# Kernel optimization log

Measured on AMD Instinct MI355X. Metric: run time of the kernel, lower is better.

The kernel has to match this reference:

```python
import jax, jax.numpy as jnp
import numpy as np

B, C, D, H, W = 8, 96, 8, 32, 32
HW, DIM, NH = H * W, C * D, 4
DH = DIM // NH
EPS_NORM = 1e-12
EPS_LN = 1e-5


def setup_inputs() -> dict:
    key = jax.random.key(0)
    ks = jax.random.split(key, 10)
    s = 0.02
    return {
        "x": jax.random.normal(ks[0], (B, C, D, H, W), jnp.float32),
        "pos_embed": jax.random.normal(ks[1], (1, HW, DIM), jnp.float32) * s,
        "qkv_w": jax.random.normal(ks[2], (3 * DIM, DIM), jnp.float32) * s,
        "proj_w": jax.random.normal(ks[3], (DIM, DIM), jnp.float32) * s,
        "proj_b": jnp.zeros((DIM,), jnp.float32),
        "temperature": jnp.ones((NH, 1, 1), jnp.float32),
        "ln_gamma": jnp.ones((DIM,), jnp.float32),
        "ln_beta": jnp.zeros((DIM,), jnp.float32),
        "dw_w": jax.random.normal(ks[4], (C, 1, 3, 3, 3), jnp.float32) * s,
        "dw_b": jnp.zeros((C,), jnp.float32),
        "pw_w": jax.random.normal(ks[5], (C, C, 1, 1, 1), jnp.float32) * s,
        "pw_b": jnp.zeros((C,), jnp.float32),
    }


def _l2norm_seq(t):
    # normalize over the HW axis (dim=-2), matching F.normalize(dim=-2)
    n = jnp.sqrt(jnp.sum(t * t, axis=-2, keepdims=True))
    return t / jnp.maximum(n, EPS_NORM)


def _dsconv(y, dw_w, dw_b, pw_w, pw_b):
    dn = ("NCDHW", "OIDHW", "NCDHW")
    z = jax.lax.conv_general_dilated(y, dw_w, (1, 1, 1), [(1, 1)] * 3,
                                     dimension_numbers=dn, feature_group_count=C)
    z = z + dw_b[None, :, None, None, None]
    z = jax.lax.conv_general_dilated(z, pw_w, (1, 1, 1), [(0, 0)] * 3,
                                     dimension_numbers=dn)
    return z + pw_b[None, :, None, None, None]


def reference(x, pos_embed, qkv_w, proj_w, proj_b, temperature,
              ln_gamma, ln_beta, dw_w, dw_b, pw_w, pw_b):
    save = x
    # b c d h w -> b (h w) (c d)
    t = jnp.transpose(x, (0, 3, 4, 1, 2)).reshape(B, HW, DIM)
    t = t + pos_embed
    # qkv projection (no bias)
    qkv = (t @ qkv_w.T).reshape(B, HW, 3, NH, DH)
    qkv = jnp.transpose(qkv, (2, 0, 3, 1, 4))  # [3,B,NH,HW,DH]
    q, k, v = qkv[0], qkv[1], qkv[2]
    q = _l2norm_seq(q)
    k = _l2norm_seq(k)
    attn = jnp.einsum("bhnd,bhmd->bhnm", q, k) * temperature  # temp broadcasts [NH,1,1]
    attn = jax.nn.softmax(attn, axis=-1)  # dropout = identity at eval
    o = jnp.einsum("bhnm,bhmd->bhnd", attn, v)
    o = jnp.transpose(o, (0, 2, 1, 3)).reshape(B, HW, DIM)
    o = o @ proj_w.T + proj_b
    # LayerNorm applied to attention output
    mu = jnp.mean(o, axis=-1, keepdims=True)
    var = jnp.mean((o - mu) ** 2, axis=-1, keepdims=True)
    o = (o - mu) / jnp.sqrt(var + EPS_LN) * ln_gamma + ln_beta
    # b (h w) (c d) -> b c d h w
    o = o.reshape(B, H, W, C, D)
    o = jnp.transpose(o, (0, 3, 4, 1, 2))
    y = o + save
    return y + _dsconv(y, dw_w, dw_b, pw_w, pw_b)
```

## Files before the change

kernel.cpp:

```cpp
#include <hip/hip_runtime.h>

typedef unsigned short u16;
typedef unsigned int u32;

typedef __attribute__((ext_vector_type(8))) short short8;
typedef __attribute__((ext_vector_type(4))) float floatx4;

__device__ __forceinline__ float bf2f(u16 u) { return __uint_as_float(((u32)u) << 16); }
__device__ __forceinline__ u16 f2bf(float f) {
    u32 x = __float_as_uint(f);
    x += 0x7fffu + ((x >> 16) & 1u);
    return (u16)(x >> 16);
}
__device__ __forceinline__ void gl_lds16(const void* g, void* l) {
    __builtin_amdgcn_global_load_lds((const __attribute__((address_space(1))) u32*)g,
                                     (__attribute__((address_space(3))) u32*)l, 16, 0, 0);
}


__global__ __launch_bounds__(256) void k_tpos(const float* __restrict__ x,
                                              const float* __restrict__ pos,
                                              u16* __restrict__ t) {
    __shared__ float tile[64][65];
    const int b = blockIdx.z, hw0 = blockIdx.y * 64, cd0 = blockIdx.x * 64;
    const int tid = threadIdx.x;
#pragma unroll
    for (int i = 0; i < 16; i++) {
        int f = i * 256 + tid;
        int cdl = f >> 6, hwl = f & 63;
        int cd = cd0 + cdl, c = cd >> 3, d = cd & 7;
        tile[cdl][hwl] = x[(size_t)(((b * 96 + c) * 8 + d)) * 1024 + hw0 + hwl];
    }
    __syncthreads();
#pragma unroll
    for (int it = 0; it < 2; it++) {
        int u = it * 256 + tid;
        int ch = u >> 6, l = u & 63;
        int n16l = ch >> 1, kcl = ch & 1;
        int hwl = n16l * 16 + (l & 15);
        int cdl = kcl * 32 + (l >> 4) * 8;
        int row = b * 1024 + hw0 + hwl;
        int cd = cd0 + cdl;
        const float* pp = pos + (size_t)(hw0 + hwl) * 768 + cd;
        float4 p0 = *(const float4*)pp;
        float4 p1 = *(const float4*)(pp + 4);
        short8 v;
        v[0] = (short)f2bf(tile[cdl + 0][hwl] + p0.x);
        v[1] = (short)f2bf(tile[cdl + 1][hwl] + p0.y);
        v[2] = (short)f2bf(tile[cdl + 2][hwl] + p0.z);
        v[3] = (short)f2bf(tile[cdl + 3][hwl] + p0.w);
        v[4] = (short)f2bf(tile[cdl + 4][hwl] + p1.x);
        v[5] = (short)f2bf(tile[cdl + 5][hwl] + p1.y);
        v[6] = (short)f2bf(tile[cdl + 6][hwl] + p1.z);
        v[7] = (short)f2bf(tile[cdl + 7][hwl] + p1.w);
        size_t chunk = (size_t)(row >> 4) * 24 + (cd >> 5);
        *(short8*)(t + chunk * 512 + l * 8) = v;
    }
}

__global__ __launch_bounds__(256) void k_cvt(const float* __restrict__ wq,
                                             const float* __restrict__ wp,
                                             const float* __restrict__ wpw,
                                             u16* __restrict__ out) {
    const int NQ = 144 * 24 * 64;
    const int NP = NQ + 48 * 24 * 64;
    int u = blockIdx.x * 256 + threadIdx.x;
    if (u < NP) {
        const float* w = (u < NQ) ? wq : wp;
        int ub = (u < NQ) ? u : u - NQ;
        int chunk = ub >> 6, l = ub & 63;
        int n16 = chunk / 24, kc = chunk - n16 * 24;
        int n = n16 * 16 + (l & 15);
        int k0 = kc * 32 + (l >> 4) * 8;
        const float* src = w + (size_t)n * 768 + k0;
        float4 a = *(const float4*)src;
        float4 b2 = *(const float4*)(src + 4);
        short8 v;
        v[0] = (short)f2bf(a.x);  v[1] = (short)f2bf(a.y);
        v[2] = (short)f2bf(a.z);  v[3] = (short)f2bf(a.w);
        v[4] = (short)f2bf(b2.x); v[5] = (short)f2bf(b2.y);
        v[6] = (short)f2bf(b2.z); v[7] = (short)f2bf(b2.w);
        *(short8*)(out + (size_t)u * 8) = v;
    } else {
        int i = u - NP;
        out[(size_t)NP * 8 + i] = f2bf(wpw[i]);
    }
}

template <int MODE>
__global__ __launch_bounds__(256) void gemm_bt(const u16* __restrict__ A,
                                               const u16* __restrict__ Bw,
                                               int M, int N, int K,
                                               u16* __restrict__ qo, u16* __restrict__ ko,
                                               u16* __restrict__ vo,
                                               const float* __restrict__ bias,
                                               float* __restrict__ Co) {
    __shared__ __align__(16) u16 lAB[32 * 512];
    u16* lA = lAB;
    u16* lB = lAB + 16 * 512;
    const int tid = threadIdx.x;
    const int lane = tid & 63;
    const int wv = tid >> 6;
    const int wr = wv >> 1, wc = wv & 1;
    const int ntiles = N >> 7;
    const int mtiles = M >> 7;
    const int lin = blockIdx.x;
    const int xcd = lin & 7;
    const int idx = lin >> 3;
    const int mlocal = idx / ntiles;
    const int ntile = idx - mlocal * ntiles;
    const int m0 = (xcd * (mtiles >> 3) + mlocal) << 7;
    const int n0 = ntile << 7;
    const int lr = lane & 15;
    const int lq = lane >> 4;

    floatx4 acc[4][4];
#pragma unroll
    for (int i = 0; i < 4; i++)
#pragma unroll
        for (int j = 0; j < 4; j++) acc[i][j] = (floatx4){0.f, 0.f, 0.f, 0.f};

    const int m16 = m0 >> 4, n16 = n0 >> 4;
    for (int kc2 = 0; kc2 < (K >> 6); kc2++) {
        __syncthreads();
#pragma unroll
        for (int kh = 0; kh < 2; kh++) {
#pragma unroll
            for (int i = 0; i < 2; i++) {
                int ch16 = i * 4 + wv;
                int kc = kc2 * 2 + kh;
                const u16* ga = A + ((size_t)(m16 + ch16) * 24 + kc) * 512 + lane * 8;
                gl_lds16(ga, (char*)lA + (kh * 8 + ch16) * 1024);
                const u16* gb = Bw + ((size_t)(n16 + ch16) * 24 + kc) * 512 + lane * 8;
                gl_lds16(gb, (char*)lB + (kh * 8 + ch16) * 1024);
            }
        }
        __syncthreads();
#pragma unroll
        for (int kh = 0; kh < 2; kh++) {
            short8 af[4], bfr[4];
#pragma unroll
            for (int tt = 0; tt < 4; tt++) {
                af[tt] = *(const short8*)(lA + ((kh * 8 + wr * 4 + tt) * 64 + lane) * 8);
                bfr[tt] = *(const short8*)(lB + ((kh * 8 + wc * 4 + tt) * 64 + lane) * 8);
            }
#pragma unroll
            for (int mt = 0; mt < 4; mt++)
#pragma unroll
                for (int nt = 0; nt < 4; nt++)
                    acc[mt][nt] = __builtin_amdgcn_mfma_f32_16x16x32_bf16(af[mt], bfr[nt], acc[mt][nt], 0, 0, 0);
        }
    }

    if (MODE == 0) {
        const int region = n0 / 768;
        const int n0r = n0 - region * 768;
        if (region == 0) {
#pragma unroll
            for (int nt = 0; nt < 4; nt++) {
                int colb = n0r + wc * 64 + nt * 16;
                int h = colb / 192;
                int dh = colb - h * 192 + lr;
#pragma unroll
                for (int mt = 0; mt < 4; mt++) {
#pragma unroll
                    for (int r = 0; r < 4; r++) {
                        int row = m0 + wr * 64 + mt * 16 + lq * 4 + r;
                        int b = row >> 10, n = row & 1023;
                        qo[((size_t)(b * 4 + h) * 1024 + n) * 192 + dh] = f2bf(acc[mt][nt][r]);
                    }
                }
            }
        } else {
            __syncthreads();
            if (region == 1) {
#pragma unroll
                for (int nt = 0; nt < 4; nt++) {
                    int lch = wc * 2 + (nt >> 1);
                    int offbase = (((nt & 1) * 2 + (lr >> 3)) * 16) * 8 + (lr & 7);
#pragma unroll
                    for (int mt = 0; mt < 4; mt++) {
                        u16* cp2 = lAB + (((wr * 4 + mt) * 4 + lch) * 512);
#pragma unroll
                        for (int r = 0; r < 4; r++)
                            cp2[offbase + (lq * 4 + r) * 8] = f2bf(acc[mt][nt][r]);
                    }
                }
            } else {
#pragma unroll
                for (int nt = 0; nt < 4; nt++) {
#pragma unroll
                    for (int mt = 0; mt < 4; mt++) {
                        u16* cp2 = lAB + (((wr * 2 + (mt >> 1)) * 8 + wc * 4 + nt) * 512);
                        int ob = (((mt & 1) * 2 + (lq >> 1)) * 16 + lr) * 8 + (lq & 1) * 4;
#pragma unroll
                        for (int r = 0; r < 4; r++)
                            cp2[ob + r] = f2bf(acc[mt][nt][r]);
                    }
                }
            }
            __syncthreads();
            const int b = m0 >> 10;
            const int ml = m0 & 1023;
#pragma unroll
            for (int i = 0; i < 8; i++) {
                int ci = wv * 8 + i;
                short8 val = *(const short8*)(lAB + ci * 512 + lane * 8);
                if (region == 1) {
                    int a = ci >> 2, bb = ci & 3;
                    int cg = n0r + bb * 32;
                    int h = cg / 192;
                    int dh32 = (cg - h * 192) >> 5;
                    size_t gaddr = (size_t)(b * 4 + h) * 196608 +
                                   (size_t)((((ml >> 4) + a) * 6 + dh32)) * 512 + lane * 8;
                    *(short8*)(ko + gaddr) = val;
                } else {
                    int a = ci >> 3, bb = ci & 7;
                    int cg = n0r + bb * 16;
                    int h = cg / 192;
                    int dh16 = (cg - h * 192) >> 4;
                    size_t gaddr = (size_t)(b * 4 + h) * 196608 +
                                   (size_t)((((ml >> 5) + a) * 12 + dh16)) * 512 + lane * 8;
                    *(short8*)(vo + gaddr) = val;
                }
            }
        }
    } else {
#pragma unroll
        for (int nt = 0; nt < 4; nt++) {
            int col = n0 + wc * 64 + nt * 16 + lr;
            float bv = bias[col];
#pragma unroll
            for (int mt = 0; mt < 4; mt++) {
#pragma unroll
                for (int r = 0; r < 4; r++) {
                    int row = m0 + wr * 64 + mt * 16 + lq * 4 + r;
                    Co[(size_t)row * N + col] = acc[mt][nt][r] + bv;
                }
            }
        }
    }
}

__global__ void k_sq(const u16* __restrict__ q, const u16* __restrict__ k,
                     float* __restrict__ sqq, float* __restrict__ sqk) {
    int bh = blockIdx.x;
    int part = blockIdx.y;
    int dh = threadIdx.x;
    const u16* qp = q + ((size_t)bh * 1024 + part * 128) * 192 + dh;
    float aq = 0.f;
#pragma unroll 4
    for (int n = 0; n < 128; n++) {
        float a = bf2f(qp[(size_t)n * 192]);
        aq += a * a;
    }
    const u16* kbase = k + (size_t)bh * 196608 + (dh >> 5) * 512 + ((dh >> 3) & 3) * 128 + (dh & 7);
    float ak = 0.f;
#pragma unroll 4
    for (int n = 0; n < 128; n++) {
        int nn = part * 128 + n;
        float c2 = bf2f(kbase[(nn >> 4) * 3072 + (nn & 15) * 8]);
        ak += c2 * c2;
    }
    atomicAdd(&sqq[bh * 192 + dh], aq);
    atomicAdd(&sqk[bh * 192 + dh], ak);
}

__global__ void k_scale(const float* __restrict__ sqq, const float* __restrict__ sqk,
                        const float* __restrict__ temp, float* __restrict__ cs) {
    int bh = blockIdx.x;
    int dh = threadIdx.x;
    float rq = 1.f / fmaxf(sqrtf(sqq[bh * 192 + dh]), 1e-12f);
    float rk = 1.f / fmaxf(sqrtf(sqk[bh * 192 + dh]), 1e-12f);
    cs[bh * 192 + dh] = rq * rk * temp[bh & 3];
}

__global__ __launch_bounds__(256) void k_attn(const u16* __restrict__ q,
                                              const u16* __restrict__ kmat,
                                              const u16* __restrict__ vT,
                                              const float* __restrict__ cs,
                                              u16* __restrict__ o) {
    __shared__ __align__(16) u16 lK[24 * 512];
    __shared__ __align__(16) u16 lV[24 * 512];
    __shared__ __align__(16) u16 lP[4 * 1024];
    const int lin = blockIdx.x;
    const int qb = (lin >> 3) & 15;
    const int bh = (lin & 7) * 4 + (lin >> 7);
    const int b = bh >> 2, h = bh & 3;
    const int tid = threadIdx.x;
    const int lane = tid & 63;
    const int wv = tid >> 6;
    const int lr = lane & 15;
    const int lq = lane >> 4;
    const int koff = lq * 8;

    const u16* qbase = q + (size_t)bh * 1024 * 192;
    const u16* kbase = kmat + (size_t)bh * 196608;
    const u16* vbase = vT + (size_t)bh * 196608;
    const float* cp = cs + bh * 192;

    const int qrow = qb * 64 + wv * 16 + lr;
    const u16* qp = qbase + (size_t)qrow * 192;
    short8 qf[6];
#pragma unroll
    for (int ks = 0; ks < 6; ks++) {
        short8 raw = *(const short8*)(qp + ks * 32 + koff);
        short8 sc;
#pragma unroll
        for (int j = 0; j < 8; j++) {
            float f = bf2f((u16)raw[j]) * cp[ks * 32 + koff + j];
            sc[j] = (short)f2bf(f);
        }
        qf[ks] = sc;
    }

    float m_r[4], l_r[4];
    floatx4 oacc[12];
#pragma unroll
    for (int r = 0; r < 4; r++) { m_r[r] = -1e30f; l_r[r] = 0.f; }
#pragma unroll
    for (int vt = 0; vt < 12; vt++) oacc[vt] = (floatx4){0.f, 0.f, 0.f, 0.f};

    u16* lp = lP + wv * 1024;

    for (int kb = 0; kb < 16; kb++) {
        __syncthreads();
#pragma unroll
        for (int i = 0; i < 6; i++) {
            int ch = i * 4 + wv;
            int ks = ch >> 2, nt = ch & 3;
            const u16* gk = kbase + ((size_t)(kb * 4 + nt) * 6 + ks) * 512 + lane * 8;
            gl_lds16(gk, (char*)lK + ch * 1024);
            int ks2 = ch / 12, vt2 = ch - ks2 * 12;
            const u16* gv = vbase + ((size_t)(kb * 2 + ks2) * 12 + vt2) * 512 + lane * 8;
            gl_lds16(gv, (char*)lV + ch * 1024);
        }
        __syncthreads();

        floatx4 s[4];
#pragma unroll
        for (int nt = 0; nt < 4; nt++) s[nt] = (floatx4){0.f, 0.f, 0.f, 0.f};
#pragma unroll
        for (int ks = 0; ks < 6; ks++) {
#pragma unroll
            for (int nt = 0; nt < 4; nt++) {
                short8 kf = *(const short8*)(lK + ((ks * 4 + nt) * 64 + lane) * 8);
                s[nt] = __builtin_amdgcn_mfma_f32_16x16x32_bf16(qf[ks], kf, s[nt], 0, 0, 0);
            }
        }

        float rmax[4];
#pragma unroll
        for (int r = 0; r < 4; r++)
            rmax[r] = fmaxf(fmaxf(s[0][r], s[1][r]), fmaxf(s[2][r], s[3][r]));
#pragma unroll
        for (int m = 1; m < 16; m <<= 1)
#pragma unroll
            for (int r = 0; r < 4; r++) rmax[r] = fmaxf(rmax[r], __shfl_xor(rmax[r], m));
        float alpha[4];
#pragma unroll
        for (int r = 0; r < 4; r++) {
            float mn = fmaxf(m_r[r], rmax[r]);
            alpha[r] = __expf(m_r[r] - mn);
            m_r[r] = mn;
        }
        float rsum[4] = {0.f, 0.f, 0.f, 0.f};
#pragma unroll
        for (int nt = 0; nt < 4; nt++)
#pragma unroll
            for (int r = 0; r < 4; r++) {
                float p = __expf(s[nt][r] - m_r[r]);
                s[nt][r] = p;
                rsum[r] += p;
            }
#pragma unroll
        for (int m = 1; m < 16; m <<= 1)
#pragma unroll
            for (int r = 0; r < 4; r++) rsum[r] += __shfl_xor(rsum[r], m);
#pragma unroll
        for (int r = 0; r < 4; r++) l_r[r] = l_r[r] * alpha[r] + rsum[r];
#pragma unroll
        for (int vt = 0; vt < 12; vt++)
#pragma unroll
            for (int r = 0; r < 4; r++) oacc[vt][r] *= alpha[r];

#pragma unroll
        for (int nt = 0; nt < 4; nt++) {
            int base2 = (nt >> 1) * 512 + ((nt & 1) * 2 + (lr >> 3)) * 128 + (lr & 7);
#pragma unroll
            for (int r = 0; r < 4; r++)
                lp[base2 + (lq * 4 + r) * 8] = f2bf(s[nt][r]);
        }

#pragma unroll
        for (int ks2 = 0; ks2 < 2; ks2++) {
            short8 pf = *(const short8*)(lp + ks2 * 512 + lane * 8);
#pragma unroll
            for (int vt = 0; vt < 12; vt++) {
                short8 vf = *(const short8*)(lV + ((ks2 * 12 + vt) * 64 + lane) * 8);
                oacc[vt] = __builtin_amdgcn_mfma_f32_16x16x32_bf16(pf, vf, oacc[vt], 0, 0, 0);
            }
        }
    }

    float inv[4];
#pragma unroll
    for (int r = 0; r < 4; r++) inv[r] = 1.f / l_r[r];
#pragma unroll
    for (int vt = 0; vt < 12; vt++) {
        int col = h * 192 + vt * 16 + lr;
#pragma unroll
        for (int r = 0; r < 4; r++) {
            int rowg = b * 1024 + qb * 64 + wv * 16 + lq * 4 + r;
            size_t addr = (size_t)(rowg >> 4) * 12288 + (col >> 5) * 512 +
                          ((col >> 3) & 3) * 128 + (rowg & 15) * 8 + (col & 7);
            o[addr] = f2bf(oacc[vt][r] * inv[r]);
        }
    }
}

__global__ __launch_bounds__(256) void k_lnstats(const float* __restrict__ o2,
                                                 float* __restrict__ mu,
                                                 float* __restrict__ rstd) {
    int row = blockIdx.x;
    int tid = threadIdx.x;
    const float* p = o2 + (size_t)row * 768;
    float s = 0.f, ss = 0.f;
    for (int i = tid; i < 768; i += 256) {
        float v = p[i];
        s += v;
        ss += v * v;
    }
#pragma unroll
    for (int m = 32; m >= 1; m >>= 1) {
        s += __shfl_xor(s, m);
        ss += __shfl_xor(ss, m);
    }
    __shared__ float as[4], ass[4];
    if ((tid & 63) == 0) {
        as[tid >> 6] = s;
        ass[tid >> 6] = ss;
    }
    __syncthreads();
    if (tid == 0) {
        float S = as[0] + as[1] + as[2] + as[3];
        float SS = ass[0] + ass[1] + ass[2] + ass[3];
        float m_ = S * (1.f / 768.f);
        float v = SS * (1.f / 768.f) - m_ * m_;
        v = fmaxf(v, 0.f);
        mu[row] = m_;
        rstd[row] = rsqrtf(v + 1e-5f);
    }
}

__global__ __launch_bounds__(256) void k_lnt(const float* __restrict__ o2,
                                             const float* __restrict__ mu,
                                             const float* __restrict__ rstd,
                                             const float* __restrict__ gamma,
                                             const float* __restrict__ beta,
                                             const float* __restrict__ x,
                                             float* __restrict__ y) {
    __shared__ float tile[64][65];
    const int b = blockIdx.z, hw0 = blockIdx.y * 64, cd0 = blockIdx.x * 64;
    const int tid = threadIdx.x;
#pragma unroll
    for (int i = 0; i < 16; i++) {
        int f = i * 256 + tid;
        int hwl = f >> 6, cdl = f & 63;
        int row = b * 1024 + hw0 + hwl;
        float v = o2[(size_t)row * 768 + cd0 + cdl];
        v = (v - mu[row]) * rstd[row] * gamma[cd0 + cdl] + beta[cd0 + cdl];
        tile[hwl][cdl] = v;
    }
    __syncthreads();
#pragma unroll
    for (int i = 0; i < 16; i++) {
        int f = i * 256 + tid;
        int cdl = f >> 6, hwl = f & 63;
        int cd = cd0 + cdl, c = cd >> 3, d = cd & 7;
        size_t addr = (size_t)((b * 96 + c) * 8 + d) * 1024 + hw0 + hwl;
        y[addr] = tile[hwl][cdl] + x[addr];
    }
}

__global__ __launch_bounds__(256) void k_dw(const float* __restrict__ y,
                                            const float* __restrict__ w,
                                            const float* __restrict__ bias,
                                            float* __restrict__ z) {
    __shared__ float ly[8192];
    const int bc = blockIdx.x;
    const int c = bc % 96;
    const int tid = threadIdx.x;
    const size_t base = (size_t)bc * 8192;

#pragma unroll
    for (int i = 0; i < 8; i++) {
        int i4 = i * 256 + tid;
        *(float4*)(ly + i4 * 4) = *(const float4*)(y + base + i4 * 4);
    }
    float wt[27];
#pragma unroll
    for (int j = 0; j < 27; j++) wt[j] = w[c * 27 + j];
    const float bv = bias[c];
    __syncthreads();

    const int wcol = tid & 31;
    const int hh = tid >> 5;

    for (int hb = 0; hb < 4; hb++) {
        const int h = hb * 8 + hh;
        float pl[3][9];
        auto loadplane = [&](int dd, float* p) {
#pragma unroll
            for (int kh = 0; kh < 3; kh++) {
                int h2 = h + kh - 1;
                bool hok = (unsigned)h2 < 32u;
                const float* row = ly + dd * 1024 + h2 * 32;
#pragma unroll
                for (int kw = 0; kw < 3; kw++) {
                    int w2 = wcol + kw - 1;
                    bool ok = hok && (unsigned)w2 < 32u;
                    p[kh * 3 + kw] = ok ? row[w2] : 0.f;
                }
            }
        };
#pragma unroll
        for (int j = 0; j < 9; j++) pl[0][j] = 0.f;
        loadplane(0, pl[1]);
#pragma unroll
        for (int d = 0; d < 8; d++) {
            if (d < 7) loadplane(d + 1, pl[2]);
            else {
#pragma unroll
                for (int j = 0; j < 9; j++) pl[2][j] = 0.f;
            }
            float acc = bv;
#pragma unroll
            for (int kd = 0; kd < 3; kd++)
#pragma unroll
                for (int j = 0; j < 9; j++) acc += wt[kd * 9 + j] * pl[kd][j];
            z[base + d * 1024 + h * 32 + wcol] = acc;
#pragma unroll
            for (int j = 0; j < 9; j++) { pl[0][j] = pl[1][j]; pl[1][j] = pl[2][j]; }
        }
    }
}

__global__ __launch_bounds__(256) void k_pw(const float* __restrict__ z,
                                            const u16* __restrict__ wbf,
                                            const float* __restrict__ bias,
                                            float* __restrict__ out) {
    __shared__ __align__(16) u16 lZ[128 * 104];
    __shared__ __align__(16) u16 lW[96 * 104];
    const int tid = threadIdx.x;
    const int lane = tid & 63;
    const int wv = tid >> 6;
    const int lr = lane & 15;
    const int lq = lane >> 4;
    const int koff = lq * 8;

    const int idx = blockIdx.x;
    const int q = idx & 7;
    const int bd = idx >> 3;
    const int b = bd >> 3, d = bd & 7;
    const int pos0 = q * 128;

    for (int i = tid; i < 96 * 96; i += 256) {
        int row = i / 96, col = i - row * 96;
        lW[row * 104 + col] = wbf[i];
    }
    {
        const int pos = tid & 127;
        const int cc0 = (tid >> 7) * 48;
        const size_t gbase = ((size_t)b * 96 * 8 + d) * 1024 + pos0 + pos;
#pragma unroll
        for (int g = 0; g < 6; g++) {
            short8 v;
#pragma unroll
            for (int j = 0; j < 8; j++) {
                int cc = cc0 + g * 8 + j;
                v[j] = (short)f2bf(z[gbase + (size_t)cc * 8192]);
            }
            *(short8*)(lZ + pos * 104 + cc0 + g * 8) = v;
        }
    }
    __syncthreads();

    floatx4 acc[6][2];
#pragma unroll
    for (int m = 0; m < 6; m++)
#pragma unroll
        for (int nt = 0; nt < 2; nt++) acc[m][nt] = (floatx4){0.f, 0.f, 0.f, 0.f};

#pragma unroll
    for (int ks = 0; ks < 3; ks++) {
        short8 bfrg[2];
#pragma unroll
        for (int nt = 0; nt < 2; nt++)
            bfrg[nt] = *(const short8*)(lZ + (wv * 32 + nt * 16 + lr) * 104 + ks * 32 + koff);
#pragma unroll
        for (int m = 0; m < 6; m++) {
            short8 afr = *(const short8*)(lW + (m * 16 + lr) * 104 + ks * 32 + koff);
#pragma unroll
            for (int nt = 0; nt < 2; nt++)
                acc[m][nt] = __builtin_amdgcn_mfma_f32_16x16x32_bf16(afr, bfrg[nt], acc[m][nt], 0, 0, 0);
        }
    }

#pragma unroll
    for (int m = 0; m < 6; m++) {
#pragma unroll
        for (int r = 0; r < 4; r++) {
            int c = m * 16 + lq * 4 + r;
            float bv = bias[c];
            size_t rowbase = ((size_t)(b * 96 + c) * 8 + d) * 1024 + pos0;
#pragma unroll
            for (int nt = 0; nt < 2; nt++) {
                int pos = wv * 32 + nt * 16 + lr;
                size_t a = rowbase + pos;
                out[a] = out[a] + bv + acc[m][nt][r];
            }
        }
    }
}

extern "C" void kernel_launch(void* const* d_in, const int* in_sizes, int n_in,
                              void* d_out, int out_size, void* d_ws, size_t ws_size,
                              hipStream_t stream) {
    (void)in_sizes; (void)n_in; (void)out_size; (void)ws_size;
    const float* x      = (const float*)d_in[0];
    const float* pos    = (const float*)d_in[1];
    const float* qkv_w  = (const float*)d_in[2];
    const float* proj_w = (const float*)d_in[3];
    const float* proj_b = (const float*)d_in[4];
    const float* temp   = (const float*)d_in[5];
    const float* ln_g   = (const float*)d_in[6];
    const float* ln_b   = (const float*)d_in[7];
    const float* dw_w   = (const float*)d_in[8];
    const float* dw_b   = (const float*)d_in[9];
    const float* pw_w   = (const float*)d_in[10];
    const float* pw_b   = (const float*)d_in[11];
    float* out = (float*)d_out;
    char* ws = (char*)d_ws;

    u16* t    = (u16*)(ws + 0);
    u16* vT   = (u16*)(ws + 12582912);
    u16* q    = (u16*)(ws + 25165824);
    u16* kk   = (u16*)(ws + 37748736);
    u16* wqb  = (u16*)(ws + 50331648);
    float* cs   = (float*)(ws + 55150592);
    float* sqq  = (float*)(ws + 55175168);
    float* sqk  = (float*)(ws + 55199744);
    float* mu   = (float*)(ws + 55224320);
    float* rstd = (float*)(ws + 55257088);
    u16* wpb  = wqb + 2304 * 768;
    u16* wpwb = wqb + 2304 * 768 + 768 * 768;
    u16* o   = t;
    float* o2 = (float*)q;
    float* z  = (float*)t;
    float* y  = out;

    k_tpos<<<dim3(12, 16, 8), 256, 0, stream>>>(x, pos, t);
    k_cvt<<<1188, 256, 0, stream>>>(qkv_w, proj_w, pw_w, wqb);
    gemm_bt<0><<<1152, 256, 0, stream>>>(t, wqb, 8192, 2304, 768, q, kk, vT, nullptr, nullptr);
    hipMemsetAsync(sqq, 0, 49152, stream);
    k_sq<<<dim3(32, 8), 192, 0, stream>>>(q, kk, sqq, sqk);
    k_scale<<<32, 192, 0, stream>>>(sqq, sqk, temp, cs);
    k_attn<<<512, 256, 0, stream>>>(q, kk, vT, cs, o);
    gemm_bt<1><<<384, 256, 0, stream>>>(o, wpb, 8192, 768, 768, nullptr, nullptr, nullptr, proj_b, o2);
    k_lnstats<<<8192, 256, 0, stream>>>(o2, mu, rstd);
    k_lnt<<<dim3(12, 16, 8), 256, 0, stream>>>(o2, mu, rstd, ln_g, ln_b, x, y);
    k_dw<<<768, 256, 0, stream>>>(y, dw_w, dw_b, z);
    k_pw<<<512, 256, 0, stream>>>(z, wpwb, pw_b, out);
}
```

Measured before the change: 295.2 us.

## Process two query tiles per wave in attention and drop online max rescaling

The attention kernel now runs with 128 threads per block, and each wave handles 32 query rows as two 16-row tiles. Every K and V fragment read from LDS therefore feeds two MFMAs, which halves LDS fragment traffic per unit of compute. The online-softmax running max and the alpha rescaling of accumulators are removed, and scores are exponentiated directly. This relies on normalized q/k keeping scores small enough not to overflow exp, which is a numerical risk if temperature or scores grow large. Register pressure rises, since two sets of accumulators are live, and fewer waves per block may reduce latency hiding.

```diff
diff --git a/kernel.cpp b/kernel.cpp
--- a/kernel.cpp
+++ b/kernel.cpp
@@ -275,14 +275,14 @@
     cs[bh * 192 + dh] = rq * rk * temp[bh & 3];
 }
 
-__global__ __launch_bounds__(256) void k_attn(const u16* __restrict__ q,
+__global__ __launch_bounds__(128) void k_attn(const u16* __restrict__ q,
                                               const u16* __restrict__ kmat,
                                               const u16* __restrict__ vT,
                                               const float* __restrict__ cs,
                                               u16* __restrict__ o) {
     __shared__ __align__(16) u16 lK[24 * 512];
     __shared__ __align__(16) u16 lV[24 * 512];
-    __shared__ __align__(16) u16 lP[4 * 1024];
+    __shared__ __align__(16) u16 lP[2 * 2048];
     const int lin = blockIdx.x;
     const int qb = (lin >> 3) & 15;
     const int bh = (lin & 7) * 4 + (lin >> 7);
@@ -299,35 +299,41 @@
     const u16* vbase = vT + (size_t)bh * 196608;
     const float* cp = cs + bh * 192;
 
-    const int qrow = qb * 64 + wv * 16 + lr;
-    const u16* qp = qbase + (size_t)qrow * 192;
-    short8 qf[6];
-#pragma unroll
-    for (int ks = 0; ks < 6; ks++) {
-        short8 raw = *(const short8*)(qp + ks * 32 + koff);
-        short8 sc;
-#pragma unroll
-        for (int j = 0; j < 8; j++) {
-            float f = bf2f((u16)raw[j]) * cp[ks * 32 + koff + j];
-            sc[j] = (short)f2bf(f);
-        }
-        qf[ks] = sc;
-    }
-
-    float m_r[4], l_r[4];
-    floatx4 oacc[12];
-#pragma unroll
-    for (int r = 0; r < 4; r++) { m_r[r] = -1e30f; l_r[r] = 0.f; }
-#pragma unroll
-    for (int vt = 0; vt < 12; vt++) oacc[vt] = (floatx4){0.f, 0.f, 0.f, 0.f};
-
-    u16* lp = lP + wv * 1024;
+    short8 qf[2][6];
+#pragma unroll
+    for (int t = 0; t < 2; t++) {
+        const int qrow = qb * 64 + wv * 32 + t * 16 + lr;
+        const u16* qp = qbase + (size_t)qrow * 192;
+#pragma unroll
+        for (int ks = 0; ks < 6; ks++) {
+            short8 raw = *(const short8*)(qp + ks * 32 + koff);
+            short8 sc;
+#pragma unroll
+            for (int j = 0; j < 8; j++) {
+                float f = bf2f((u16)raw[j]) * cp[ks * 32 + koff + j];
+                sc[j] = (short)f2bf(f);
+            }
+            qf[t][ks] = sc;
+        }
+    }
+
+    float l_r[2][4];
+    floatx4 oacc[2][12];
+#pragma unroll
+    for (int t = 0; t < 2; t++) {
+#pragma unroll
+        for (int r = 0; r < 4; r++) l_r[t][r] = 0.f;
+#pragma unroll
+        for (int vt = 0; vt < 12; vt++) oacc[t][vt] = (floatx4){0.f, 0.f, 0.f, 0.f};
+    }
+
+    u16* lp = lP + wv * 2048;
 
     for (int kb = 0; kb < 16; kb++) {
         __syncthreads();
 #pragma unroll
-        for (int i = 0; i < 6; i++) {
-            int ch = i * 4 + wv;
+        for (int i = 0; i < 12; i++) {
+            int ch = i * 2 + wv;
             int ks = ch >> 2, nt = ch & 3;
             const u16* gk = kbase + ((size_t)(kb * 4 + nt) * 6 + ks) * 512 + lane * 8;
             gl_lds16(gk, (char*)lK + ch * 1024);
@@ -337,84 +343,84 @@
         }
         __syncthreads();
 
-        floatx4 s[4];
-#pragma unroll
-        for (int nt = 0; nt < 4; nt++) s[nt] = (floatx4){0.f, 0.f, 0.f, 0.f};
+        floatx4 s0[4], s1[4];
+#pragma unroll
+        for (int nt = 0; nt < 4; nt++) {
+            s0[nt] = (floatx4){0.f, 0.f, 0.f, 0.f};
+            s1[nt] = (floatx4){0.f, 0.f, 0.f, 0.f};
+        }
 #pragma unroll
         for (int ks = 0; ks < 6; ks++) {
 #pragma unroll
             for (int nt = 0; nt < 4; nt++) {
                 short8 kf = *(const short8*)(lK + ((ks * 4 + nt) * 64 + lane) * 8);
-                s[nt] = __builtin_amdgcn_mfma_f32_16x16x32_bf16(qf[ks], kf, s[nt], 0, 0, 0);
-            }
-        }
-
-        float rmax[4];
-#pragma unroll
-        for (int r = 0; r < 4; r++)
-            rmax[r] = fmaxf(fmaxf(s[0][r], s[1][r]), fmaxf(s[2][r], s[3][r]));
+                s0[nt] = __builtin_amdgcn_mfma_f32_16x16x32_bf16(qf[0][ks], kf, s0[nt], 0, 0, 0);
+                s1[nt] = __builtin_amdgcn_mfma_f32_16x16x32_bf16(qf[1][ks], kf, s1[nt], 0, 0, 0);
+            }
+        }
+
+        float rs0[4] = {0.f, 0.f, 0.f, 0.f}, rs1[4] = {0.f, 0.f, 0.f, 0.f};
+#pragma unroll
+        for (int nt = 0; nt < 4; nt++)
+#pragma unroll
+            for (int r = 0; r < 4; r++) {
+                float p0 = __expf(s0[nt][r]);
+                s0[nt][r] = p0;
+                rs0[r] += p0;
+                float p1 = __expf(s1[nt][r]);
+                s1[nt][r] = p1;
+                rs1[r] += p1;
+            }
 #pragma unroll
         for (int m = 1; m < 16; m <<= 1)
 #pragma unroll
-            for (int r = 0; r < 4; r++) rmax[r] = fmaxf(rmax[r], __shfl_xor(rmax[r], m));
-        float alpha[4];
+            for (int r = 0; r < 4; r++) {
+                rs0[r] += __shfl_xor(rs0[r], m);
+                rs1[r] += __shfl_xor(rs1[r], m);
+            }
 #pragma unroll
         for (int r = 0; r < 4; r++) {
-            float mn = fmaxf(m_r[r], rmax[r]);
-            alpha[r] = __expf(m_r[r] - mn);
-            m_r[r] = mn;
-        }
-        float rsum[4] = {0.f, 0.f, 0.f, 0.f};
-#pragma unroll
-        for (int nt = 0; nt < 4; nt++)
-#pragma unroll
-            for (int r = 0; r < 4; r++) {
-                float p = __expf(s[nt][r] - m_r[r]);
-                s[nt][r] = p;
-                rsum[r] += p;
-            }
-#pragma unroll
-        for (int m = 1; m < 16; m <<= 1)
-#pragma unroll
-            for (int r = 0; r < 4; r++) rsum[r] += __shfl_xor(rsum[r], m);
-#pragma unroll
-        for (int r = 0; r < 4; r++) l_r[r] = l_r[r] * alpha[r] + rsum[r];
-#pragma unroll
-        for (int vt = 0; vt < 12; vt++)
-#pragma unroll
-            for (int r = 0; r < 4; r++) oacc[vt][r] *= alpha[r];
-
+            l_r[0][r] += rs0[r];
+            l_r[1][r] += rs1[r];
+        }
 #pragma unroll
         for (int nt = 0; nt < 4; nt++) {
             int base2 = (nt >> 1) * 512 + ((nt & 1) * 2 + (lr >> 3)) * 128 + (lr & 7);
 #pragma unroll
-            for (int r = 0; r < 4; r++)
-                lp[base2 + (lq * 4 + r) * 8] = f2bf(s[nt][r]);
+            for (int r = 0; r < 4; r++) {
+                lp[base2 + (lq * 4 + r) * 8] = f2bf(s0[nt][r]);
+                lp[1024 + base2 + (lq * 4 + r) * 8] = f2bf(s1[nt][r]);
+            }
         }
 
 #pragma unroll
         for (int ks2 = 0; ks2 < 2; ks2++) {
-            short8 pf = *(const short8*)(lp + ks2 * 512 + lane * 8);
+            short8 pf0 = *(const short8*)(lp + ks2 * 512 + lane * 8);
+            short8 pf1 = *(const short8*)(lp + 1024 + ks2 * 512 + lane * 8);
 #pragma unroll
             for (int vt = 0; vt < 12; vt++) {
                 short8 vf = *(const short8*)(lV + ((ks2 * 12 + vt) * 64 + lane) * 8);
-                oacc[vt] = __builtin_amdgcn_mfma_f32_16x16x32_bf16(pf, vf, oacc[vt], 0, 0, 0);
-            }
-        }
-    }
-
-    float inv[4];
-#pragma unroll
-    for (int r = 0; r < 4; r++) inv[r] = 1.f / l_r[r];
-#pragma unroll
-    for (int vt = 0; vt < 12; vt++) {
-        int col = h * 192 + vt * 16 + lr;
-#pragma unroll
-        for (int r = 0; r < 4; r++) {
-            int rowg = b * 1024 + qb * 64 + wv * 16 + lq * 4 + r;
-            size_t addr = (size_t)(rowg >> 4) * 12288 + (col >> 5) * 512 +
-                          ((col >> 3) & 3) * 128 + (rowg & 15) * 8 + (col & 7);
-            o[addr] = f2bf(oacc[vt][r] * inv[r]);
+                oacc[0][vt] = __builtin_amdgcn_mfma_f32_16x16x32_bf16(pf0, vf, oacc[0][vt], 0, 0, 0);
+                oacc[1][vt] = __builtin_amdgcn_mfma_f32_16x16x32_bf16(pf1, vf, oacc[1][vt], 0, 0, 0);
+            }
+        }
+    }
+
+#pragma unroll
+    for (int t = 0; t < 2; t++) {
+        float inv[4];
+#pragma unroll
+        for (int r = 0; r < 4; r++) inv[r] = 1.f / l_r[t][r];
+#pragma unroll
+        for (int vt = 0; vt < 12; vt++) {
+            int col = h * 192 + vt * 16 + lr;
+#pragma unroll
+            for (int r = 0; r < 4; r++) {
+                int rowg = b * 1024 + qb * 64 + wv * 32 + t * 16 + lq * 4 + r;
+                size_t addr = (size_t)(rowg >> 4) * 12288 + (col >> 5) * 512 +
+                              ((col >> 3) & 3) * 128 + (rowg & 15) * 8 + (col & 7);
+                o[addr] = f2bf(oacc[t][vt][r] * inv[r]);
+            }
         }
     }
 }
@@ -666,7 +672,7 @@
     hipMemsetAsync(sqq, 0, 49152, stream);
     k_sq<<<dim3(32, 8), 192, 0, stream>>>(q, kk, sqq, sqk);
     k_scale<<<32, 192, 0, stream>>>(sqq, sqk, temp, cs);
-    k_attn<<<512, 256, 0, stream>>>(q, kk, vT, cs, o);
+    k_attn<<<512, 128, 0, stream>>>(q, kk, vT, cs, o);
     gemm_bt<1><<<384, 256, 0, stream>>>(o, wpb, 8192, 768, 768, nullptr, nullptr, nullptr, proj_b, o2);
     k_lnstats<<<8192, 256, 0, stream>>>(o2, mu, rstd);
     k_lnt<<<dim3(12, 16, 8), 256, 0, stream>>>(o2, mu, rstd, ln_g, ln_b, x, y);
```

Result: faster. 288.8 us (-2.2%).
